# Performance work log

Hardware: AMD Instinct MI355X
Metric: run time of the kernel (lower is better)

The kernel has to match this reference:

```python
import jax, jax.numpy as jnp
import numpy as np

# Scalar quantization params (QLinear __init__ args)
FEATURE_BITWIDTH = 8
WEIGHT_BITWIDTH = 8
INPUT_ZERO_POINT = -3
OUTPUT_ZERO_POINT = -5
INPUT_SCALE = 0.05
OUTPUT_SCALE = 0.1
QMIN = -(1 << (FEATURE_BITWIDTH - 1))   # -128
QMAX = (1 << (FEATURE_BITWIDTH - 1)) - 1  # 127

M, K, N = 8192, 4096, 4096


def float_to_fixed_point(x, bitwidth):
    """Represent x (0 < x < 1) as int_scale * 2^-frac_bits with int_scale
    in [2^(bitwidth-2), 2^(bitwidth-1)) (mantissa fits in signed `bitwidth` bits)."""
    frac_bits = (bitwidth - 1 - jnp.ceil(jnp.log2(x))).astype(jnp.int32)
    int_scale = jnp.round(x * jnp.exp2(frac_bits.astype(jnp.float32))).astype(jnp.int32)
    return int_scale, frac_bits


def setup_inputs() -> dict:
    key = jax.random.key(0)
    k1, k2, k3, k4 = jax.random.split(key, 4)
    qinput = jax.random.randint(k1, (M, K), -128, 128, dtype=jnp.int8)
    qweight = jax.random.randint(k2, (N, K), -128, 128, dtype=jnp.int8)
    qbias = jax.random.randint(k3, (N,), -(1 << 16), 1 << 16, dtype=jnp.int32)
    # per-output-channel weight scale; keeps folded scale in (0, 1)
    weight_scale = jax.random.uniform(k4, (N,), jnp.float32, 0.002, 0.02)
    return {"qinput": qinput, "qweight": qweight, "qbias": qbias,
            "weight_scale": weight_scale}


def reference(qinput, qweight, qbias, weight_scale):
    w32 = qweight.astype(jnp.int32)                      # [N, K]
    # Qbias' = qbias - sum_k(qweight) * Zin  (bias shift folding input zero point)
    shifted_qbias = qbias - w32.sum(axis=1) * INPUT_ZERO_POINT  # [N]
    # int32 GEMM: [M, K] @ [K, N] + bias
    acc = qinput.astype(jnp.int32) @ w32.T + shifted_qbias[None, :]  # [M, N]
    # fixed-point requantization: (acc * int_scale) >> frac_bits + Zout
    folded_scale = INPUT_SCALE * weight_scale / OUTPUT_SCALE         # [N], in (0,1)
    int_scale, frac_bits = float_to_fixed_point(folded_scale, FEATURE_BITWIDTH)
    # widen to int64 for the multiply so the (acc * int_scale) product cannot wrap
    prod = acc.astype(jnp.int64) * int_scale.astype(jnp.int64)[None, :]
    scaled = jnp.right_shift(prod, frac_bits.astype(jnp.int64)[None, :])  # arithmetic >>
    out = scaled + OUTPUT_ZERO_POINT
    return jnp.clip(out, QMIN, QMAX).astype(jnp.int8)
```

## Files before the change

### kernel.cpp

```cpp
#include <hip/hip_runtime.h>
#include <cstdint>
#include <cstddef>

#define M_DIM 8192
#define N_DIM 4096
#define K_DIM 4096

#define BM 128
#define BN 128
#define BK 128

#define BM2 256
#define BN2 256
#define BK2 128
#define NKT (K_DIM / BK2)

typedef int int32x4  __attribute__((ext_vector_type(4)));
typedef int int32x16 __attribute__((ext_vector_type(16)));


typedef __attribute__((address_space(1))) const void* gas_cptr;
typedef __attribute__((address_space(3))) void* las_ptr;

__device__ __forceinline__ void async_copy16(const void* g, void* l) {
    __builtin_amdgcn_global_load_lds((gas_cptr)g, (las_ptr)l, 16, 0, 0);
}

__device__ __forceinline__ int32x4 pack16(const int* p) {
    const int32x4* v = (const int32x4*)p;
    int32x4 w0 = v[0], w1 = v[1], w2 = v[2], w3 = v[3];
    int32x4 r;
    r.x = (w0.x & 0xFF) | ((w0.y & 0xFF) << 8) | ((w0.z & 0xFF) << 16) | (w0.w << 24);
    r.y = (w1.x & 0xFF) | ((w1.y & 0xFF) << 8) | ((w1.z & 0xFF) << 16) | (w1.w << 24);
    r.z = (w2.x & 0xFF) | ((w2.y & 0xFF) << 8) | ((w2.z & 0xFF) << 16) | (w2.w << 24);
    r.w = (w3.x & 0xFF) | ((w3.y & 0xFF) << 8) | ((w3.z & 0xFF) << 16) | (w3.w << 24);
    return r;
}

__global__ void ql_detect_kernel(const int* a, const int* b, int* ws) {
    int t = threadIdx.x;
    int fa = 0, fb = 0;
    for (int i = t; i < 4096; i += 64) {
        int va = a[i]; if (va > 127 || va < -128) fa = 1;
        int vb = b[i]; if (vb > 127 || vb < -128) fb = 1;
    }
    unsigned long long ba = __ballot(fa);
    unsigned long long bb = __ballot(fb);
    if (t == 0) { ws[0] = ba ? 1 : 0; ws[1] = bb ? 1 : 0; }
}

__global__ __launch_bounds__(256)
void ql_pack2_kernel(const void* wsrc, int* wdst, const void* asrc, int* adst,
                     const int* ws, long ndwW, long ndwA) {
    const int fA = __builtin_amdgcn_readfirstlane(ws[0]);
    const int fW = __builtin_amdgcn_readfirstlane(ws[1]);
    const long nW = fW ? 0 : ndwW;
    const long nA = fA ? 0 : ndwA;
    const long total = nW + nA;
    const long stride = (long)gridDim.x * 256;
    for (long c = (long)blockIdx.x * 256 + threadIdx.x; c < total; c += stride) {
        if (c < nW) {
            int32x4 v = ((const int32x4*)wsrc)[c];
            wdst[c] = (v.x & 0xFF) | ((v.y & 0xFF) << 8) | ((v.z & 0xFF) << 16) | (v.w << 24);
        } else {
            const long ca = c - nW;
            int32x4 v = ((const int32x4*)asrc)[ca];
            adst[ca] = (v.x & 0xFF) | ((v.y & 0xFF) << 8) | ((v.z & 0xFF) << 16) | (v.w << 24);
        }
    }
}

__global__ void ql_prep8_kernel(const void* worig, const int8_t* w8p, const int* qbias,
                                const float* wscale, int* ws) {
    const int fb = __builtin_amdgcn_readfirstlane(ws[1]);
    const int8_t* w8 = fb ? (const int8_t*)worig : w8p;

    const int lane = threadIdx.x & 63;
    const int wid  = threadIdx.x >> 6;
    const int n = blockIdx.x * 4 + wid;

    const int32x4* row = (const int32x4*)(w8 + (size_t)n * K_DIM);
    int s = 0;
    for (int c = lane; c < K_DIM / 16; c += 64) {
        int32x4 v = row[c];
#pragma unroll
        for (int j = 0; j < 4; ++j) {
            int w = (j == 0) ? v.x : (j == 1) ? v.y : (j == 2) ? v.z : v.w;
            s += (int)(int8_t)(w) + (int)(int8_t)(w >> 8)
               + (int)(int8_t)(w >> 16) + (w >> 24);
        }
    }
#pragma unroll
    for (int off = 32; off > 0; off >>= 1) s += __shfl_down(s, off, 64);

    if (lane == 0) {
        ws[16 + n] = qbias[n] + 3 * s;
        float folded = (0.05f * wscale[n]) / 0.1f;
        int fbits = (int)(7.0f - ceilf(log2f(folded)));
        int isc = (int)rintf(folded * exp2f((float)fbits));
        ws[16 + N_DIM + n] = isc;
        ws[16 + 2 * N_DIM + n] = fbits;
    }
}

__global__ void ql_prep_kernel(const void* wptr, const int* qbias,
                               const float* wscale, int* ws) {
    const int lane = threadIdx.x & 63;
    const int wid  = threadIdx.x >> 6;
    const int n = blockIdx.x * 4 + wid;
    const int b8 = __builtin_amdgcn_readfirstlane(ws[1]);

    int s = 0;
    if (b8) {
        const int32x4* row = (const int32x4*)((const int8_t*)wptr + (size_t)n * K_DIM);
        for (int c = lane; c < K_DIM / 16; c += 64) {
            int32x4 v = row[c];
#pragma unroll
            for (int j = 0; j < 4; ++j) {
                int w = (j == 0) ? v.x : (j == 1) ? v.y : (j == 2) ? v.z : v.w;
                s += (int)(int8_t)(w) + (int)(int8_t)(w >> 8)
                   + (int)(int8_t)(w >> 16) + (w >> 24);
            }
        }
    } else {
        const int32x4* row = (const int32x4*)((const int*)wptr + (size_t)n * K_DIM);
        for (int c = lane; c < K_DIM / 4; c += 64) {
            int32x4 v = row[c];
            s += v.x + v.y + v.z + v.w;
        }
    }
#pragma unroll
    for (int off = 32; off > 0; off >>= 1) s += __shfl_down(s, off, 64);

    if (lane == 0) {
        ws[16 + n] = qbias[n] + 3 * s;
        float folded = (0.05f * wscale[n]) / 0.1f;
        int fbits = (int)(7.0f - ceilf(log2f(folded)));
        int isc = (int)rintf(folded * exp2f((float)fbits));
        ws[16 + N_DIM + n] = isc;
        ws[16 + 2 * N_DIM + n] = fbits;
    }
}

__device__ __forceinline__ void ql_epilogue(int32x4 acc[4][4], const int* ws,
                                            int* out, int bm, int bn,
                                            int wm, int wn, int qm, int qh) {
    const int* qb  = ws + 16;
    const int* isc = ws + 16 + N_DIM;
    const int* fbt = ws + 16 + 2 * N_DIM;
#pragma unroll
    for (int j = 0; j < 4; ++j) {
        const int n_g = bn * BN + wn + j * 16 + qm;
        const int b0 = qb[n_g];
        const int s0 = isc[n_g];
        const int f0 = fbt[n_g];
#pragma unroll
        for (int i = 0; i < 4; ++i) {
            const int m_base = bm * BM + wm + i * 16 + qh * 4;
#pragma unroll
            for (int r = 0; r < 4; ++r) {
                int v = ((r == 0) ? acc[i][j].x : (r == 1) ? acc[i][j].y
                        : (r == 2) ? acc[i][j].z : acc[i][j].w) + b0;
                long long p = (long long)v * (long long)s0;
                int o = (int)(p >> f0) - 5;
                o = o < -128 ? -128 : (o > 127 ? 127 : o);
                out[(size_t)(m_base + r) * N_DIM + n_g] = o;
            }
        }
    }
}


#define LOAD_AF(BUF, MH) do { \
    _Pragma("unroll") for (int ml = 0; ml < 2; ++ml) \
    _Pragma("unroll") for (int kc = 0; kc < 4; ++kc) \
        af[ml][kc] = LA[BUF][baseAe[kc] + (MH) * 512 + ml * 256]; \
} while (0)

#define LOAD_BF(BUF, NH, DST) do { \
    _Pragma("unroll") for (int kc = 0; kc < 4; ++kc) \
        DST[kc] = LB[BUF][baseBe[kc] + (NH) * 256]; \
} while (0)

#define MFMA_QUAD(MH, NH, BF) do { \
    __builtin_amdgcn_s_setprio(1); \
    _Pragma("unroll") for (int kc = 0; kc < 4; ++kc) \
    _Pragma("unroll") for (int ml = 0; ml < 2; ++ml) \
        acc[(MH) * 2 + ml][NH] = __builtin_amdgcn_mfma_i32_32x32x32_i8( \
            af[ml][kc], BF[kc], acc[(MH) * 2 + ml][NH], 0, 0, 0); \
    __builtin_amdgcn_s_setprio(0); \
} while (0)

#define STAGE_A(BUF, H, TT) do { \
    async_copy16(gA + (size_t)(TT) * 128 + (H) * 524288,          &LA[BUF][(H) * 1024 + t]); \
    async_copy16(gA + (size_t)(TT) * 128 + (H) * 524288 + 262144, &LA[BUF][(H) * 1024 + 512 + t]); \
} while (0)

#define STAGE_B(BUF, H, TT) do { \
    async_copy16(gB + (size_t)(TT) * 128 + (H) * 524288,          &LB[BUF][(H) * 1024 + t]); \
    async_copy16(gB + (size_t)(TT) * 128 + (H) * 524288 + 262144, &LB[BUF][(H) * 1024 + 512 + t]); \
} while (0)

#define TILE_BODY(BUF, TT, VMC) do { \
    asm volatile("s_waitcnt vmcnt(" #VMC ")"); \
    __builtin_amdgcn_s_barrier(); \
    LOAD_AF(BUF, 0); \
    LOAD_BF(BUF, 0, bf0); \
    if ((TT) + 1 < NKT) { STAGE_A(BUF ^ 1, 1, (TT) + 1); } \
    __builtin_amdgcn_s_barrier(); \
    MFMA_QUAD(0, 0, bf0); \
    __builtin_amdgcn_s_barrier(); \
    LOAD_BF(BUF, 1, bf1); \
    if ((TT) + 1 < NKT) { STAGE_B(BUF ^ 1, 1, (TT) + 1); } \
    __builtin_amdgcn_s_barrier(); \
    MFMA_QUAD(0, 1, bf1); \
    __builtin_amdgcn_s_barrier(); \
    LOAD_AF(BUF, 1); \
    if ((TT) + 2 < NKT) { STAGE_B(BUF, 0, (TT) + 2); } \
    __builtin_amdgcn_s_barrier(); \
    MFMA_QUAD(1, 0, bf0); \
    __builtin_amdgcn_s_barrier(); \
    if ((TT) + 2 < NKT) { STAGE_A(BUF, 0, (TT) + 2); } \
    __builtin_amdgcn_s_barrier(); \
    MFMA_QUAD(1, 1, bf1); \
} while (0)

__global__ __launch_bounds__(512, 2)
void ql_gemm8_kernel(const void* a0, const int8_t* a8,
                     const void* b0, const int8_t* w8,
                     const int* ws, int* out) {
    __shared__ int32x4 LA[2][2048];
    __shared__ int32x4 LB[2][2048];

    const int fa = __builtin_amdgcn_readfirstlane(ws[0]);
    const int fb = __builtin_amdgcn_readfirstlane(ws[1]);
    const int8_t* aptr = fa ? (const int8_t*)a0 : a8;
    const int8_t* bptr = fb ? (const int8_t*)b0 : w8;

    const int t    = threadIdx.x;
    const int lane = t & 63;
    const int wid  = t >> 6;
    const int wr   = wid >> 2;
    const int wc   = wid & 3;
    const int l31  = lane & 31;
    const int hi   = lane >> 5;

    const int bn = blockIdx.x;
    const int bm = blockIdx.y;
    const int arow0 = bm * BM2;
    const int brow0 = bn * BN2;

    int baseAe[4], baseBe[4];
#pragma unroll
    for (int kc = 0; kc < 4; ++kc) {
        const int phys = (kc * 2 + hi) ^ (lane & 7);
        baseAe[kc] = (wr * 128 + l31) * 8 + phys;
        baseBe[kc] = (wc * 64  + l31) * 8 + phys;
    }

    const int colg = (t & 7) ^ ((t >> 3) & 7);
    const int8_t* gA = aptr + (size_t)(arow0 + (t >> 3)) * K_DIM + colg * 16;
    const int8_t* gB = bptr + (size_t)(brow0 + (t >> 3)) * K_DIM + colg * 16;

    int32x16 acc[4][2] = {};
    int32x4 af[2][4], bf0[4], bf1[4];

    STAGE_A(0, 0, 0); STAGE_B(0, 0, 0);
    STAGE_A(0, 1, 0); STAGE_B(0, 1, 0);
    STAGE_A(1, 0, 1); STAGE_B(1, 0, 1);

#pragma unroll 1
    for (int T = 0; T < NKT - 4; T += 2) {
        TILE_BODY(0, T, 4);
        TILE_BODY(1, T + 1, 4);
    }
    TILE_BODY(0, NKT - 4, 4);
    TILE_BODY(1, NKT - 3, 4);
    TILE_BODY(0, NKT - 2, 4);
    TILE_BODY(1, NKT - 1, 0);

    const int* qb  = ws + 16;
    const int* isc = ws + 16 + N_DIM;
    const int* fbt = ws + 16 + 2 * N_DIM;
#pragma unroll
    for (int j = 0; j < 2; ++j) {
        const int n_g = bn * BN2 + wc * 64 + j * 32 + l31;
        const int b0r = qb[n_g];
        const int s0r = isc[n_g];
        const int f0r = fbt[n_g];
#pragma unroll
        for (int i = 0; i < 4; ++i) {
            const int m0 = bm * BM2 + wr * 128 + i * 32 + hi * 4;
#pragma unroll
            for (int reg = 0; reg < 16; ++reg) {
                const int row = (reg & 3) + 8 * (reg >> 2);
                int v = acc[i][j][reg] + b0r;
                long long p = (long long)v * (long long)s0r;
                int o = (int)(p >> f0r) - 5;
                o = o < -128 ? -128 : (o > 127 ? 127 : o);
                out[(size_t)(m0 + row) * N_DIM + n_g] = o;
            }
        }
    }
}

__global__ __launch_bounds__(256)
void ql_gemm_fb_kernel(const void* aptr, const void* bptr, const int* ws, int* out) {
    __shared__ int32x4 Als[BM * BK / 16];
    __shared__ int32x4 Bls[BN * BK / 16];

    const int a8 = __builtin_amdgcn_readfirstlane(ws[0]);
    const int b8 = __builtin_amdgcn_readfirstlane(ws[1]);

    const int t    = threadIdx.x;
    const int lane = t & 63;
    const int wid  = t >> 6;
    const int bn = blockIdx.x;
    const int bm = blockIdx.y;

    const int wm = (wid >> 1) * 64;
    const int wn = (wid & 1) * 64;
    const int qm = lane & 15;
    const int qh = lane >> 4;

    int32x4 acc[4][4] = {};

    for (int kt = 0; kt < K_DIM / BK; ++kt) {
        __syncthreads();
        const int k0 = kt * BK;
#pragma unroll
        for (int r = 0; r < 4; ++r) {
            const int c    = r * 256 + t;
            const int row  = c >> 3;
            const int colg = (c & 7) ^ (row & 7);
            const size_t offA = (size_t)(bm * BM + row) * K_DIM + k0 + colg * 16;
            const size_t offB = (size_t)(bn * BN + row) * K_DIM + k0 + colg * 16;
            if (a8) async_copy16((const int8_t*)aptr + offA, &Als[c]);
            else    Als[c] = pack16((const int*)aptr + offA);
            if (b8) async_copy16((const int8_t*)bptr + offB, &Bls[c]);
            else    Bls[c] = pack16((const int*)bptr + offB);
        }
        __syncthreads();

#pragma unroll
        for (int s = 0; s < 2; ++s) {
            const int colk = s * 4 + qh;
            int32x4 af[4], bf[4];
#pragma unroll
            for (int i = 0; i < 4; ++i) {
                const int ra = wm + i * 16 + qm;
                const int rb = wn + i * 16 + qm;
                af[i] = Als[ra * 8 + (colk ^ (ra & 7))];
                bf[i] = Bls[rb * 8 + (colk ^ (rb & 7))];
            }
#pragma unroll
            for (int i = 0; i < 4; ++i)
#pragma unroll
                for (int j = 0; j < 4; ++j)
                    acc[i][j] = __builtin_amdgcn_mfma_i32_16x16x64_i8(
                        af[i], bf[j], acc[i][j], 0, 0, 0);
        }
    }
    ql_epilogue(acc, ws, out, bm, bn, wm, wn, qm, qh);
}

extern "C" void kernel_launch(void* const* d_in, const int* in_sizes, int n_in,
                              void* d_out, int out_size, void* d_ws, size_t ws_size,
                              hipStream_t stream) {
    const void* qin    = d_in[0];
    const void* qwt    = d_in[1];
    const int* qbias   = (const int*)d_in[2];
    const float* wscal = (const float*)d_in[3];
    int* ws  = (int*)d_ws;
    int* out = (int*)d_out;

    hipLaunchKernelGGL(ql_detect_kernel, dim3(1), dim3(64), 0, stream,
                       (const int*)qin, (const int*)qwt, ws);

    const size_t need = 65536 + (size_t)M_DIM * K_DIM + (size_t)N_DIM * K_DIM;
    if (ws_size >= need) {
        int8_t* a8 = (int8_t*)d_ws + 65536;
        int8_t* w8 = a8 + (size_t)M_DIM * K_DIM;
        const long ndwA = (long)M_DIM * K_DIM / 4;
        const long ndwW = (long)N_DIM * K_DIM / 4;
        const long ndwT = ndwA + ndwW;
        hipLaunchKernelGGL(ql_pack2_kernel, dim3((unsigned)(ndwT / (256 * 4))), dim3(256),
                           0, stream, qwt, (int*)w8, qin, (int*)a8, ws, ndwW, ndwA);
        hipLaunchKernelGGL(ql_prep8_kernel, dim3(N_DIM / 4), dim3(256), 0, stream,
                           qwt, w8, qbias, wscal, ws);
        hipLaunchKernelGGL(ql_gemm8_kernel, dim3(N_DIM / BN2, M_DIM / BM2), dim3(512),
                           0, stream, qin, a8, qwt, w8, ws, out);
    } else {
        hipLaunchKernelGGL(ql_prep_kernel, dim3(N_DIM / 4), dim3(256), 0, stream,
                           qwt, qbias, wscal, ws);
        hipLaunchKernelGGL(ql_gemm_fb_kernel, dim3(N_DIM / BN, M_DIM / BM), dim3(256), 0, stream,
                           qin, qwt, ws, out);
    }
}
```

Baseline: 426.1 us.

## Replace eight-barrier interleaved tile schedule with simple double-buffered load-all-then-MFMA loop

Replaces the fine-grained schedule, which had eight barriers per K-tile and staged half-tiles two steps ahead, with a plain double buffer. Each tile now loads all A and B fragments from LDS, issues the full next-tile async copies, runs 32 MFMAs, then does one __syncthreads. The LDS XOR swizzle also gains an extra term based on row group, meant to cut bank conflicts. This lowers barrier overhead but prefetches only one tile ahead, raises register pressure from holding all fragments, and relies on __syncthreads draining the async copies.

```diff
diff --git a/kernel.cpp b/kernel.cpp
--- a/kernel.cpp
+++ b/kernel.cpp
@@ -171,58 +171,40 @@
 }
 
 
-#define LOAD_AF(BUF, MH) do { \
-    _Pragma("unroll") for (int ml = 0; ml < 2; ++ml) \
-    _Pragma("unroll") for (int kc = 0; kc < 4; ++kc) \
-        af[ml][kc] = LA[BUF][baseAe[kc] + (MH) * 512 + ml * 256]; \
-} while (0)
-
-#define LOAD_BF(BUF, NH, DST) do { \
-    _Pragma("unroll") for (int kc = 0; kc < 4; ++kc) \
-        DST[kc] = LB[BUF][baseBe[kc] + (NH) * 256]; \
-} while (0)
-
-#define MFMA_QUAD(MH, NH, BF) do { \
+#define TILE2(BUF, TT) do { \
+    _Pragma("unroll") for (int ml = 0; ml < 2; ++ml) \
+    _Pragma("unroll") for (int kc = 0; kc < 4; ++kc) \
+        afL[ml][kc] = LA[BUF][baseAe[kc] + ml * 256]; \
+    _Pragma("unroll") for (int kc = 0; kc < 4; ++kc) \
+        bf0[kc] = LB[BUF][baseBe[kc]]; \
+    _Pragma("unroll") for (int kc = 0; kc < 4; ++kc) \
+        bf1[kc] = LB[BUF][baseBe[kc] + 256]; \
+    _Pragma("unroll") for (int ml = 0; ml < 2; ++ml) \
+    _Pragma("unroll") for (int kc = 0; kc < 4; ++kc) \
+        afH[ml][kc] = LA[BUF][baseAe[kc] + 512 + ml * 256]; \
+    if ((TT) + 1 < NKT) { \
+        _Pragma("unroll") for (int h2 = 0; h2 < 4; ++h2) { \
+            async_copy16(gA + (size_t)((TT) + 1) * 128 + (size_t)h2 * 262144, \
+                         &LA[(BUF) ^ 1][h2 * 512 + t]); \
+            async_copy16(gB + (size_t)((TT) + 1) * 128 + (size_t)h2 * 262144, \
+                         &LB[(BUF) ^ 1][h2 * 512 + t]); \
+        } \
+    } \
     __builtin_amdgcn_s_setprio(1); \
     _Pragma("unroll") for (int kc = 0; kc < 4; ++kc) \
     _Pragma("unroll") for (int ml = 0; ml < 2; ++ml) \
-        acc[(MH) * 2 + ml][NH] = __builtin_amdgcn_mfma_i32_32x32x32_i8( \
-            af[ml][kc], BF[kc], acc[(MH) * 2 + ml][NH], 0, 0, 0); \
+        acc[ml][0] = __builtin_amdgcn_mfma_i32_32x32x32_i8(afL[ml][kc], bf0[kc], acc[ml][0], 0, 0, 0); \
+    _Pragma("unroll") for (int kc = 0; kc < 4; ++kc) \
+    _Pragma("unroll") for (int ml = 0; ml < 2; ++ml) \
+        acc[ml][1] = __builtin_amdgcn_mfma_i32_32x32x32_i8(afL[ml][kc], bf1[kc], acc[ml][1], 0, 0, 0); \
+    _Pragma("unroll") for (int kc = 0; kc < 4; ++kc) \
+    _Pragma("unroll") for (int ml = 0; ml < 2; ++ml) \
+        acc[2 + ml][0] = __builtin_amdgcn_mfma_i32_32x32x32_i8(afH[ml][kc], bf0[kc], acc[2 + ml][0], 0, 0, 0); \
+    _Pragma("unroll") for (int kc = 0; kc < 4; ++kc) \
+    _Pragma("unroll") for (int ml = 0; ml < 2; ++ml) \
+        acc[2 + ml][1] = __builtin_amdgcn_mfma_i32_32x32x32_i8(afH[ml][kc], bf1[kc], acc[2 + ml][1], 0, 0, 0); \
     __builtin_amdgcn_s_setprio(0); \
-} while (0)
-
-#define STAGE_A(BUF, H, TT) do { \
-    async_copy16(gA + (size_t)(TT) * 128 + (H) * 524288,          &LA[BUF][(H) * 1024 + t]); \
-    async_copy16(gA + (size_t)(TT) * 128 + (H) * 524288 + 262144, &LA[BUF][(H) * 1024 + 512 + t]); \
-} while (0)
-
-#define STAGE_B(BUF, H, TT) do { \
-    async_copy16(gB + (size_t)(TT) * 128 + (H) * 524288,          &LB[BUF][(H) * 1024 + t]); \
-    async_copy16(gB + (size_t)(TT) * 128 + (H) * 524288 + 262144, &LB[BUF][(H) * 1024 + 512 + t]); \
-} while (0)
-
-#define TILE_BODY(BUF, TT, VMC) do { \
-    asm volatile("s_waitcnt vmcnt(" #VMC ")"); \
-    __builtin_amdgcn_s_barrier(); \
-    LOAD_AF(BUF, 0); \
-    LOAD_BF(BUF, 0, bf0); \
-    if ((TT) + 1 < NKT) { STAGE_A(BUF ^ 1, 1, (TT) + 1); } \
-    __builtin_amdgcn_s_barrier(); \
-    MFMA_QUAD(0, 0, bf0); \
-    __builtin_amdgcn_s_barrier(); \
-    LOAD_BF(BUF, 1, bf1); \
-    if ((TT) + 1 < NKT) { STAGE_B(BUF ^ 1, 1, (TT) + 1); } \
-    __builtin_amdgcn_s_barrier(); \
-    MFMA_QUAD(0, 1, bf1); \
-    __builtin_amdgcn_s_barrier(); \
-    LOAD_AF(BUF, 1); \
-    if ((TT) + 2 < NKT) { STAGE_B(BUF, 0, (TT) + 2); } \
-    __builtin_amdgcn_s_barrier(); \
-    MFMA_QUAD(1, 0, bf0); \
-    __builtin_amdgcn_s_barrier(); \
-    if ((TT) + 2 < NKT) { STAGE_A(BUF, 0, (TT) + 2); } \
-    __builtin_amdgcn_s_barrier(); \
-    MFMA_QUAD(1, 1, bf1); \
+    __syncthreads(); \
 } while (0)
 
 __global__ __launch_bounds__(512, 2)
@@ -250,34 +232,34 @@
     const int arow0 = bm * BM2;
     const int brow0 = bn * BN2;
 
+    const int fr = (lane & 7) ^ ((l31 >> 3) & 3);
     int baseAe[4], baseBe[4];
 #pragma unroll
     for (int kc = 0; kc < 4; ++kc) {
-        const int phys = (kc * 2 + hi) ^ (lane & 7);
+        const int phys = (kc * 2 + hi) ^ fr;
         baseAe[kc] = (wr * 128 + l31) * 8 + phys;
         baseBe[kc] = (wc * 64  + l31) * 8 + phys;
     }
 
-    const int colg = (t & 7) ^ ((t >> 3) & 7);
+    const int colg = (t & 7) ^ ((t >> 3) & 7) ^ ((t >> 6) & 3);
     const int8_t* gA = aptr + (size_t)(arow0 + (t >> 3)) * K_DIM + colg * 16;
     const int8_t* gB = bptr + (size_t)(brow0 + (t >> 3)) * K_DIM + colg * 16;
 
     int32x16 acc[4][2] = {};
-    int32x4 af[2][4], bf0[4], bf1[4];
-
-    STAGE_A(0, 0, 0); STAGE_B(0, 0, 0);
-    STAGE_A(0, 1, 0); STAGE_B(0, 1, 0);
-    STAGE_A(1, 0, 1); STAGE_B(1, 0, 1);
+    int32x4 afL[2][4], afH[2][4], bf0[4], bf1[4];
+
+#pragma unroll
+    for (int h2 = 0; h2 < 4; ++h2) {
+        async_copy16(gA + (size_t)h2 * 262144, &LA[0][h2 * 512 + t]);
+        async_copy16(gB + (size_t)h2 * 262144, &LB[0][h2 * 512 + t]);
+    }
+    __syncthreads();
 
 #pragma unroll 1
-    for (int T = 0; T < NKT - 4; T += 2) {
-        TILE_BODY(0, T, 4);
-        TILE_BODY(1, T + 1, 4);
-    }
-    TILE_BODY(0, NKT - 4, 4);
-    TILE_BODY(1, NKT - 3, 4);
-    TILE_BODY(0, NKT - 2, 4);
-    TILE_BODY(1, NKT - 1, 0);
+    for (int T = 0; T < NKT; T += 2) {
+        TILE2(0, T);
+        TILE2(1, T + 1);
+    }
 
     const int* qb  = ws + 16;
     const int* isc = ws + 16 + N_DIM;
```

Result: faster. 414.4 us (-2.7%).
